# Optimization experiments

Measured on AMD Instinct MI355X. Metric: run time of the kernel, lower is better.

## Reference

```python
import jax, jax.numpy as jnp
import numpy as np
from jax import lax

B, L, LQ, D_IN, ET, H, INIT_EMBED = 16, 256, 64, 32, 128, 4, 8
DIM = 2 * D_IN          # attention value/feature dim (x concat mask)
ETK = ET // H           # per-head time-embedding dim


def _lin(key, fan_in, shape):
    b = 1.0 / np.sqrt(fan_in)
    return jax.random.uniform(key, shape, jnp.float32, -b, b)


def setup_inputs() -> dict:
    key = jax.random.key(0)
    ks = jax.random.split(key, 24)
    inp = {
        "x": jax.random.normal(ks[0], (B, L, D_IN), jnp.float32),
        "time_steps": jnp.sort(jax.random.uniform(ks[1], (B, L), jnp.float32), axis=-1),
        "mask": (jax.random.uniform(ks[2], (B, L, D_IN)) > 0.5).astype(jnp.float32),
        "query": jnp.linspace(0.0, 1.0, LQ, dtype=jnp.float32),
        # time embedding: Linear(1,1) and Linear(1, ET-1)
        "w_lin": _lin(ks[3], 1, (1,)), "b_lin": _lin(ks[4], 1, (1,)),
        "w_per": _lin(ks[5], 1, (ET - 1,)), "b_per": _lin(ks[6], 1, (ET - 1,)),
        # attention projections (stored as (in,out))
        "Wq": _lin(ks[7], ET, (ET, ET)), "bq": _lin(ks[8], ET, (ET,)),
        "Wk": _lin(ks[9], ET, (ET, ET)), "bk": _lin(ks[10], ET, (ET,)),
        "Wo": _lin(ks[11], H * DIM, (H * DIM, ET)), "bo": _lin(ks[12], H * DIM, (ET,)),
        # vanilla RNN (tanh)
        "W_ih": _lin(ks[13], ET, (ET, ET)), "b_ih": _lin(ks[14], ET, (ET,)),
        "W_hh": _lin(ks[15], ET, (ET, ET)), "b_hh": _lin(ks[16], ET, (ET,)),
        "r1_w": _lin(ks[17], ET, (ET, 128)), "r1_b": _lin(ks[17], ET, (128,)),
        "r2_w": _lin(ks[18], 128, (128, 128)), "r2_b": _lin(ks[18], 128, (128,)),
        "r3_w": _lin(ks[19], 128, (128, ET)), "r3_b": _lin(ks[19], 128, (ET,)),
        "r4_w": _lin(ks[20], ET, (ET, INIT_EMBED)), "r4_b": _lin(ks[20], ET, (INIT_EMBED,)),
    }
    return inp


def reference(x, time_steps, mask, query,
              w_lin, b_lin, w_per, b_per,
              Wq, bq, Wk, bk, Wo, bo,
              W_ih, b_ih, W_hh, b_hh,
              r1_w, r1_b, r2_w, r2_b, r3_w, r3_b, r4_w, r4_b):
    def time_embed(tt):  # (...,) -> (..., ET)
        tt = tt[..., None]
        return jnp.concatenate([tt * w_lin + b_lin,
                                jnp.sin(tt * w_per + b_per)], axis=-1)

    xc = jnp.concatenate([x, mask], axis=-1)          # (B,L,DIM) value
    m2 = jnp.concatenate([mask, mask], axis=-1)       # (B,L,DIM)

    kemb = time_embed(time_steps)                     # (B,L,ET)
    qemb = time_embed(query)                          # (LQ,ET)

    q = (qemb @ Wq + bq).reshape(LQ, H, ETK).transpose(1, 0, 2)       # (H,LQ,ETK)
    k = (kemb @ Wk + bk).reshape(B, L, H, ETK).transpose(0, 2, 1, 3)  # (B,H,L,ETK)

    scores = jnp.einsum('hqe,bhke->bhqk', q, k) / np.sqrt(ETK)        # (B,H,LQ,L)
    # per-feature mask broadcast: (B,H,LQ,L,DIM)
    s5 = jnp.where(m2[:, None, None, :, :] == 0, -1e9, scores[..., None])
    p = jax.nn.softmax(s5, axis=-2)                   # softmax over keys L
    att = jnp.einsum('bhqkd,bkd->bhqd', p, xc)        # (B,H,LQ,DIM)
    att = att.transpose(0, 2, 1, 3).reshape(B, LQ, H * DIM)
    out = att @ Wo + bo                               # (B,LQ,ET)

    # vanilla tanh RNN, return final hidden state
    def step(h, xt):
        h = jnp.tanh(xt @ W_ih + b_ih + h @ W_hh + b_hh)
        return h, None
    h0 = jnp.zeros((B, ET), out.dtype)
    hT, _ = lax.scan(step, h0, out.transpose(1, 0, 2))  # scan over LQ

    y = hT @ r1_w + r1_b
    y = y @ r2_w + r2_b
    y = y @ r3_w + r3_b
    y = y @ r4_w + r4_b                               # (B, INIT_EMBED)
    return y
```

## Files before the change

kernel.cpp:

```cpp
#include <hip/hip_runtime.h>
#include <hip/hip_bf16.h>


#define NB 16
#define NL 256
#define NLQ 64
#define NDIN 32
#define NET 128
#define NH 4
#define NETK 32

#define HPAD 136
#define PAD(i) ((i) + 4 * ((i) >> 6))

typedef float f32x2 __attribute__((ext_vector_type(2)));

__global__ __launch_bounds__(128) void k_embed_proj(
    const float* __restrict__ ts, const float* __restrict__ query,
    const float* __restrict__ mask,
    const float* __restrict__ w_lin, const float* __restrict__ b_lin,
    const float* __restrict__ w_per, const float* __restrict__ b_per,
    const float* __restrict__ Wk, const float* __restrict__ bk,
    const float* __restrict__ Wq, const float* __restrict__ bq,
    float* __restrict__ kproj, float* __restrict__ qproj,
    unsigned* __restrict__ mbg) {
  __shared__ __align__(16) float emb[8 * NET];
  int g = blockIdx.x;
  int j = threadIdx.x;
  if (g >= 520) {
    int b = g - 520;
#pragma unroll
    for (int half = 0; half < 2; half++) {
      int r = j + 128 * half;
      const float4* mr4 = (const float4*)(mask + (size_t)(b * NL + r) * NDIN);
      unsigned bits = 0;
#pragma unroll
      for (int u = 0; u < 8; u++) {
        float4 m = mr4[u];
        bits |= (m.x != 0.f ? 1u : 0u) << (4 * u);
        bits |= (m.y != 0.f ? 1u : 0u) << (4 * u + 1);
        bits |= (m.z != 0.f ? 1u : 0u) << (4 * u + 2);
        bits |= (m.w != 0.f ? 1u : 0u) << (4 * u + 3);
      }
      mbg[b * NL + r] = bits;
    }
    return;
  }
  bool isQ = (g >= 512);
  int base = (isQ ? g - 512 : g) * 8;
  float wl_ = w_lin[0], bl_ = b_lin[0];
  float wp = (j > 0) ? w_per[j - 1] : 0.f;
  float bp = (j > 0) ? b_per[j - 1] : 0.f;
#pragma unroll
  for (int rr = 0; rr < 8; rr++) {
    float t = isQ ? query[base + rr] : ts[base + rr];
    emb[rr * NET + j] = (j == 0) ? (t * wl_ + bl_) : sinf(t * wp + bp);
  }
  __syncthreads();
  const float* W = isQ ? Wq : Wk;
  float bias = isQ ? bq[j] : bk[j];
  float acc[8];
#pragma unroll
  for (int rr = 0; rr < 8; rr++) acc[rr] = bias;
#pragma unroll 2
  for (int i = 0; i < NET; i += 4) {
    float w0 = W[(size_t)i * NET + j];
    float w1 = W[(size_t)(i + 1) * NET + j];
    float w2 = W[(size_t)(i + 2) * NET + j];
    float w3 = W[(size_t)(i + 3) * NET + j];
#pragma unroll
    for (int rr = 0; rr < 8; rr++) {
      float4 e4 = *(const float4*)&emb[rr * NET + i];
      acc[rr] += e4.x * w0 + e4.y * w1 + e4.z * w2 + e4.w * w3;
    }
  }
  float* dst = isQ ? qproj : kproj;
#pragma unroll
  for (int rr = 0; rr < 8; rr++) dst[(size_t)(base + rr) * NET + j] = acc[rr];
}

__global__ __launch_bounds__(256) void k_attn(
    const float* __restrict__ x, const unsigned* __restrict__ mbg,
    const float* __restrict__ qproj, const float* __restrict__ kproj,
    float* __restrict__ att) {
  const float SC = 0.17677669529663687f;
  int blk = blockIdx.x;
  int qg = blk & 15;
  int h  = (blk >> 4) & 3;
  int b  = blk >> 6;
  int t  = threadIdx.x;

  __shared__ __align__(16) float es4[NL * 4];
  __shared__ float part[3 * 32 * 9];

  {
    int k = t;
    float kr[NETK];
    const float4* kp =
        (const float4*)(kproj + (size_t)(b * NL + k) * NET + h * NETK);
#pragma unroll
    for (int i = 0; i < 8; i++) {
      float4 v = kp[i];
      kr[4 * i] = v.x; kr[4 * i + 1] = v.y;
      kr[4 * i + 2] = v.z; kr[4 * i + 3] = v.w;
    }
    float ev[4];
#pragma unroll
    for (int qq = 0; qq < 4; qq++) {
      const float* qv = qproj + (size_t)(qg * 4 + qq) * NET + h * NETK;
      float s0 = 0.f, s1 = 0.f;
#pragma unroll
      for (int i = 0; i < NETK; i += 2) {
        s0 += qv[i] * kr[i];
        s1 += qv[i + 1] * kr[i + 1];
      }
      ev[qq] = __expf((s0 + s1) * SC);
    }
    *(float4*)&es4[k * 4] = make_float4(ev[0], ev[1], ev[2], ev[3]);
  }
  __syncthreads();

  int kq = t >> 5, c = t & 31;
  f32x2 den01 = {0.f, 0.f}, den23 = {0.f, 0.f};
  f32x2 num01 = {0.f, 0.f}, num23 = {0.f, 0.f};
  float sumx = 0.f;
  {
    const float* xb = x + (size_t)b * NL * NDIN;
    const unsigned* mbb = mbg + b * NL;
    int k0 = kq * 32;
#pragma unroll 4
    for (int kk = 0; kk < 32; kk++) {
      int k = k0 + kk;
      float4 e4 = *(const float4*)&es4[k * 4];
      float xv = xb[(size_t)k * NDIN + c];
      float mv = ((mbb[k] >> c) & 1u) ? 1.f : 0.f;
      sumx += xv;
      f32x2 e01 = (f32x2){e4.x, e4.y} * mv;
      f32x2 e23 = (f32x2){e4.z, e4.w} * mv;
      den01 += e01;
      den23 += e23;
      num01 += e01 * xv;
      num23 += e23 * xv;
    }
  }
  float den[4] = {den01.x, den01.y, den23.x, den23.y};
  float num[4] = {num01.x, num01.y, num23.x, num23.y};
  sumx += __shfl_xor(sumx, 32, 64);
#pragma unroll
  for (int q = 0; q < 4; q++) {
    den[q] += __shfl_xor(den[q], 32, 64);
    num[q] += __shfl_xor(num[q], 32, 64);
  }
  {
    int w = t >> 6, lane = t & 63;
    if (w > 0 && lane < 32) {
      float* p = &part[((w - 1) * 32 + c) * 9];
#pragma unroll
      for (int q = 0; q < 4; q++) { p[q] = den[q]; p[4 + q] = num[q]; }
      p[8] = sumx;
    }
  }
  __syncthreads();

  if (t < 32) {
#pragma unroll
    for (int ww = 0; ww < 3; ww++) {
      const float* p = &part[(ww * 32 + t) * 9];
#pragma unroll
      for (int q = 0; q < 4; q++) { den[q] += p[q]; num[q] += p[4 + q]; }
      sumx += p[8];
    }
    float meanx = sumx * (1.f / 256.f);
#pragma unroll
    for (int qq = 0; qq < 4; qq++) {
      bool any = (den[qq] > 0.f);
      float* ao =
          att + (size_t)(((b * NLQ + qg * 4 + qq) * NH) + h) * 64;
      ao[t]      = any ? (num[qq] / den[qq]) : meanx;
      ao[32 + t] = any ? 1.f : 0.f;
    }
  }
}

__global__ __launch_bounds__(128) void k_out_xw(
    const float* __restrict__ att,
    const float* __restrict__ Wo, const float* __restrict__ bo,
    const float* __restrict__ Wih, const float* __restrict__ bih,
    const float* __restrict__ bhh, float* __restrict__ XW) {
  int r = blockIdx.x;
  int j = threadIdx.x;
  __shared__ __align__(16) float arow[NH * 64];
  __shared__ __align__(16) float orow[NET];
  arow[j]       = att[(size_t)r * 256 + j];
  arow[j + 128] = att[(size_t)r * 256 + 128 + j];
  __syncthreads();
  float a0 = bo[j], a1 = 0.f, a2 = 0.f, a3 = 0.f;
#pragma unroll 4
  for (int u = 0; u < 256; u += 4) {
    float4 av = *(const float4*)&arow[u];
    a0 += av.x * Wo[(size_t)u * NET + j];
    a1 += av.y * Wo[(size_t)(u + 1) * NET + j];
    a2 += av.z * Wo[(size_t)(u + 2) * NET + j];
    a3 += av.w * Wo[(size_t)(u + 3) * NET + j];
  }
  orow[j] = (a0 + a1) + (a2 + a3);
  __syncthreads();
  float b0 = bih[j] + bhh[j], b1 = 0.f, b2 = 0.f, b3 = 0.f;
#pragma unroll 4
  for (int e = 0; e < NET; e += 4) {
    float4 ov = *(const float4*)&orow[e];
    b0 += ov.x * Wih[(size_t)e * NET + j];
    b1 += ov.y * Wih[(size_t)(e + 1) * NET + j];
    b2 += ov.z * Wih[(size_t)(e + 2) * NET + j];
    b3 += ov.w * Wih[(size_t)(e + 3) * NET + j];
  }
  XW[(size_t)r * NET + j] = (b0 + b1) + (b2 + b3);
}

__device__ __forceinline__ void layer128(const float* src_lds,
                                         const float* __restrict__ W,
                                         const float* __restrict__ bvec,
                                         float* dst_lds, int j, int s) {
  const float4* h4 = (const float4*)(src_lds + s * 68);
  float a0 = 0.f, a1 = 0.f, a2 = 0.f, a3 = 0.f;
#pragma unroll
  for (int i = 0; i < 16; i++) {
    float4 hv = h4[i];
    int base = (s * 64 + 4 * i) * NET + j;
    a0 += hv.x * W[base];
    a1 += hv.y * W[base + NET];
    a2 += hv.z * W[base + 2 * NET];
    a3 += hv.w * W[base + 3 * NET];
  }
  float acc = (a0 + a1) + (a2 + a3);
  acc += __shfl_xor(acc, 1, 64);
  if (s == 0) dst_lds[PAD(j)] = acc + bvec[j];
}

__global__ __launch_bounds__(256, 1) void k_rnn(
    const float* __restrict__ XW, const float* __restrict__ Whh,
    const float* __restrict__ r1w, const float* __restrict__ r1b,
    const float* __restrict__ r2w, const float* __restrict__ r2b,
    const float* __restrict__ r3w, const float* __restrict__ r3b,
    const float* __restrict__ r4w, const float* __restrict__ r4b,
    float* __restrict__ out) {
  int b = blockIdx.x;
  int tid = threadIdx.x;
  int s = tid & 1;
  int j = tid >> 1;
  __shared__ float xwl[NLQ * NET];
  __shared__ float hb[2][HPAD];
  __shared__ float tmp[HPAD];
  {
    const float4* src = (const float4*)(XW + (size_t)b * NLQ * NET);
    float4* dst = (float4*)xwl;
#pragma unroll
    for (int u = 0; u < 8; u++) dst[tid + 256 * u] = src[tid + 256 * u];
  }
  f32x2 w2[32];
#pragma unroll
  for (int i = 0; i < 32; i++) {
    w2[i].x = Whh[(s * 64 + 2 * i) * NET + j];
    w2[i].y = Whh[(s * 64 + 2 * i + 1) * NET + j];
  }
  if (tid < 128) hb[0][PAD(tid)] = 0.f;
  __syncthreads();
  for (int t = 0; t < NLQ; t++) {
    float xwv = xwl[t * NET + j];
    const float4* h4 = (const float4*)&hb[t & 1][s * 68];
    f32x2 accA = {0.f, 0.f}, accB = {0.f, 0.f};
#pragma unroll
    for (int i = 0; i < 16; i++) {
      float4 hv = h4[i];
      accA += (f32x2){hv.x, hv.y} * w2[2 * i];
      accB += (f32x2){hv.z, hv.w} * w2[2 * i + 1];
    }
    float acc = (accA.x + accA.y) + (accB.x + accB.y);
    acc += __shfl_xor(acc, 1, 64);
    if (s == 0) {
      float z = acc + xwv;
      float e2 = __expf(2.f * z);
      hb[(t + 1) & 1][PAD(j)] = 1.f - 2.f / (e2 + 1.f);
    }
    __syncthreads();
  }
  layer128(hb[0], r1w, r1b, tmp, j, s);
  __syncthreads();
  layer128(tmp, r2w, r2b, hb[1], j, s);
  __syncthreads();
  layer128(hb[1], r3w, r3b, hb[0], j, s);
  __syncthreads();
  if (tid < 64) {
    int jj = tid >> 3, p = tid & 7;
    float y = 0.f;
#pragma unroll
    for (int i = 0; i < 16; i++) {
      int ii = p * 16 + i;
      y += hb[0][PAD(ii)] * r4w[ii * 8 + jj];
    }
    y += __shfl_xor(y, 1, 64);
    y += __shfl_xor(y, 2, 64);
    y += __shfl_xor(y, 4, 64);
    if (p == 0) out[b * 8 + jj] = y + r4b[jj];
  }
}

extern "C" void kernel_launch(void* const* d_in, const int* in_sizes, int n_in,
                              void* d_out, int out_size, void* d_ws, size_t ws_size,
                              hipStream_t stream) {
  const float* x     = (const float*)d_in[0];
  const float* ts    = (const float*)d_in[1];
  const float* mask  = (const float*)d_in[2];
  const float* query = (const float*)d_in[3];
  const float* w_lin = (const float*)d_in[4];
  const float* b_lin = (const float*)d_in[5];
  const float* w_per = (const float*)d_in[6];
  const float* b_per = (const float*)d_in[7];
  const float* Wq    = (const float*)d_in[8];
  const float* bq    = (const float*)d_in[9];
  const float* Wk    = (const float*)d_in[10];
  const float* bk    = (const float*)d_in[11];
  const float* Wo    = (const float*)d_in[12];
  const float* bo    = (const float*)d_in[13];
  const float* Wih   = (const float*)d_in[14];
  const float* bih   = (const float*)d_in[15];
  const float* Whh   = (const float*)d_in[16];
  const float* bhh   = (const float*)d_in[17];
  const float* r1w   = (const float*)d_in[18];
  const float* r1b   = (const float*)d_in[19];
  const float* r2w   = (const float*)d_in[20];
  const float* r2b   = (const float*)d_in[21];
  const float* r3w   = (const float*)d_in[22];
  const float* r3b   = (const float*)d_in[23];
  const float* r4w   = (const float*)d_in[24];
  const float* r4b   = (const float*)d_in[25];
  float* out = (float*)d_out;

  float* ws    = (float*)d_ws;
  float* kproj = ws;
  float* qproj = ws + 524288;
  float* att   = ws + 532480;
  float* XW    = ws + 794624;
  unsigned* mbg = (unsigned*)(ws + 925696);

  k_embed_proj<<<536, 128, 0, stream>>>(
      ts, query, mask, w_lin, b_lin, w_per, b_per, Wk, bk, Wq, bq,
      kproj, qproj, mbg);
  k_attn<<<NB * NH * 16, 256, 0, stream>>>(x, mbg, qproj, kproj, att);
  k_out_xw<<<NB * NLQ, 128, 0, stream>>>(att, Wo, bo, Wih, bih, bhh, XW);
  k_rnn<<<NB, 256, 0, stream>>>(XW, Whh, r1w, r1b, r2w, r2b, r3w, r3b,
                                r4w, r4b, out);
}
```

Before: 173.3 us.

## Use packed f32x2 FMA in projections and split RNN step over four lanes

Rewrites the dot-product inner loops of the projection, attention-score and output/input-weight kernels to use two-wide float vector accumulators, which can map to packed FMA instructions. The recurrent kernel moves from 256 to 512 threads, so each hidden unit's recurrent dot product is split across four lanes with 32 weights each instead of two lanes with 64, and the partial sums are combined with an extra shuffle. The aim is to shorten the serial per-timestep latency of the 64-step recurrence. In exchange there is one more shuffle per step, a barrier across twice as many threads each step, and the regressor layers now run on half the block while the rest idles.

```diff
diff --git a/kernel.cpp b/kernel.cpp
--- a/kernel.cpp
+++ b/kernel.cpp
@@ -59,24 +59,24 @@
   __syncthreads();
   const float* W = isQ ? Wq : Wk;
   float bias = isQ ? bq[j] : bk[j];
-  float acc[8];
-#pragma unroll
-  for (int rr = 0; rr < 8; rr++) acc[rr] = bias;
+  f32x2 acc2[8];
+#pragma unroll
+  for (int rr = 0; rr < 8; rr++) acc2[rr] = (f32x2){bias, 0.f};
 #pragma unroll 2
   for (int i = 0; i < NET; i += 4) {
-    float w0 = W[(size_t)i * NET + j];
-    float w1 = W[(size_t)(i + 1) * NET + j];
-    float w2 = W[(size_t)(i + 2) * NET + j];
-    float w3 = W[(size_t)(i + 3) * NET + j];
+    f32x2 wA = {W[(size_t)i * NET + j], W[(size_t)(i + 1) * NET + j]};
+    f32x2 wB = {W[(size_t)(i + 2) * NET + j], W[(size_t)(i + 3) * NET + j]};
 #pragma unroll
     for (int rr = 0; rr < 8; rr++) {
       float4 e4 = *(const float4*)&emb[rr * NET + i];
-      acc[rr] += e4.x * w0 + e4.y * w1 + e4.z * w2 + e4.w * w3;
+      acc2[rr] += (f32x2){e4.x, e4.y} * wA;
+      acc2[rr] += (f32x2){e4.z, e4.w} * wB;
     }
   }
   float* dst = isQ ? qproj : kproj;
 #pragma unroll
-  for (int rr = 0; rr < 8; rr++) dst[(size_t)(base + rr) * NET + j] = acc[rr];
+  for (int rr = 0; rr < 8; rr++)
+    dst[(size_t)(base + rr) * NET + j] = acc2[rr].x + acc2[rr].y;
 }
 
 __global__ __launch_bounds__(256) void k_attn(
@@ -108,13 +108,11 @@
 #pragma unroll
     for (int qq = 0; qq < 4; qq++) {
       const float* qv = qproj + (size_t)(qg * 4 + qq) * NET + h * NETK;
-      float s0 = 0.f, s1 = 0.f;
-#pragma unroll
-      for (int i = 0; i < NETK; i += 2) {
-        s0 += qv[i] * kr[i];
-        s1 += qv[i + 1] * kr[i + 1];
-      }
-      ev[qq] = __expf((s0 + s1) * SC);
+      f32x2 s2 = {0.f, 0.f};
+#pragma unroll
+      for (int i = 0; i < NETK; i += 2)
+        s2 += (f32x2){qv[i], qv[i + 1]} * (f32x2){kr[i], kr[i + 1]};
+      ev[qq] = __expf((s2.x + s2.y) * SC);
     }
     *(float4*)&es4[k * 4] = make_float4(ev[0], ev[1], ev[2], ev[3]);
   }
@@ -194,27 +192,27 @@
   arow[j]       = att[(size_t)r * 256 + j];
   arow[j + 128] = att[(size_t)r * 256 + 128 + j];
   __syncthreads();
-  float a0 = bo[j], a1 = 0.f, a2 = 0.f, a3 = 0.f;
+  f32x2 A = {bo[j], 0.f}, B = {0.f, 0.f};
 #pragma unroll 4
   for (int u = 0; u < 256; u += 4) {
     float4 av = *(const float4*)&arow[u];
-    a0 += av.x * Wo[(size_t)u * NET + j];
-    a1 += av.y * Wo[(size_t)(u + 1) * NET + j];
-    a2 += av.z * Wo[(size_t)(u + 2) * NET + j];
-    a3 += av.w * Wo[(size_t)(u + 3) * NET + j];
-  }
-  orow[j] = (a0 + a1) + (a2 + a3);
-  __syncthreads();
-  float b0 = bih[j] + bhh[j], b1 = 0.f, b2 = 0.f, b3 = 0.f;
+    A += (f32x2){av.x, av.y} *
+         (f32x2){Wo[(size_t)u * NET + j], Wo[(size_t)(u + 1) * NET + j]};
+    B += (f32x2){av.z, av.w} *
+         (f32x2){Wo[(size_t)(u + 2) * NET + j], Wo[(size_t)(u + 3) * NET + j]};
+  }
+  orow[j] = (A.x + A.y) + (B.x + B.y);
+  __syncthreads();
+  f32x2 C = {bih[j] + bhh[j], 0.f}, D = {0.f, 0.f};
 #pragma unroll 4
   for (int e = 0; e < NET; e += 4) {
     float4 ov = *(const float4*)&orow[e];
-    b0 += ov.x * Wih[(size_t)e * NET + j];
-    b1 += ov.y * Wih[(size_t)(e + 1) * NET + j];
-    b2 += ov.z * Wih[(size_t)(e + 2) * NET + j];
-    b3 += ov.w * Wih[(size_t)(e + 3) * NET + j];
-  }
-  XW[(size_t)r * NET + j] = (b0 + b1) + (b2 + b3);
+    C += (f32x2){ov.x, ov.y} *
+         (f32x2){Wih[(size_t)e * NET + j], Wih[(size_t)(e + 1) * NET + j]};
+    D += (f32x2){ov.z, ov.w} *
+         (f32x2){Wih[(size_t)(e + 2) * NET + j], Wih[(size_t)(e + 3) * NET + j]};
+  }
+  XW[(size_t)r * NET + j] = (C.x + C.y) + (D.x + D.y);
 }
 
 __device__ __forceinline__ void layer128(const float* src_lds,
@@ -237,7 +235,7 @@
   if (s == 0) dst_lds[PAD(j)] = acc + bvec[j];
 }
 
-__global__ __launch_bounds__(256, 1) void k_rnn(
+__global__ __launch_bounds__(512, 1) void k_rnn(
     const float* __restrict__ XW, const float* __restrict__ Whh,
     const float* __restrict__ r1w, const float* __restrict__ r1b,
     const float* __restrict__ r2w, const float* __restrict__ r2b,
@@ -246,8 +244,8 @@
     float* __restrict__ out) {
   int b = blockIdx.x;
   int tid = threadIdx.x;
-  int s = tid & 1;
-  int j = tid >> 1;
+  int s = tid & 3;
+  int j = tid >> 2;
   __shared__ float xwl[NLQ * NET];
   __shared__ float hb[2][HPAD];
   __shared__ float tmp[HPAD];
@@ -255,28 +253,31 @@
     const float4* src = (const float4*)(XW + (size_t)b * NLQ * NET);
     float4* dst = (float4*)xwl;
 #pragma unroll
-    for (int u = 0; u < 8; u++) dst[tid + 256 * u] = src[tid + 256 * u];
-  }
-  f32x2 w2[32];
-#pragma unroll
-  for (int i = 0; i < 32; i++) {
-    w2[i].x = Whh[(s * 64 + 2 * i) * NET + j];
-    w2[i].y = Whh[(s * 64 + 2 * i + 1) * NET + j];
+    for (int u = 0; u < 4; u++) dst[tid + 512 * u] = src[tid + 512 * u];
+  }
+  int qoff = s * 32;
+  f32x2 w2[16];
+#pragma unroll
+  for (int i = 0; i < 16; i++) {
+    w2[i].x = Whh[(size_t)(qoff + 2 * i) * NET + j];
+    w2[i].y = Whh[(size_t)(qoff + 2 * i + 1) * NET + j];
   }
   if (tid < 128) hb[0][PAD(tid)] = 0.f;
   __syncthreads();
+  int loff = qoff + 4 * (s >> 1);
   for (int t = 0; t < NLQ; t++) {
     float xwv = xwl[t * NET + j];
-    const float4* h4 = (const float4*)&hb[t & 1][s * 68];
+    const float4* h4 = (const float4*)&hb[t & 1][loff];
     f32x2 accA = {0.f, 0.f}, accB = {0.f, 0.f};
 #pragma unroll
-    for (int i = 0; i < 16; i++) {
+    for (int i = 0; i < 8; i++) {
       float4 hv = h4[i];
       accA += (f32x2){hv.x, hv.y} * w2[2 * i];
       accB += (f32x2){hv.z, hv.w} * w2[2 * i + 1];
     }
     float acc = (accA.x + accA.y) + (accB.x + accB.y);
     acc += __shfl_xor(acc, 1, 64);
+    acc += __shfl_xor(acc, 2, 64);
     if (s == 0) {
       float z = acc + xwv;
       float e2 = __expf(2.f * z);
@@ -284,11 +285,12 @@
     }
     __syncthreads();
   }
-  layer128(hb[0], r1w, r1b, tmp, j, s);
-  __syncthreads();
-  layer128(tmp, r2w, r2b, hb[1], j, s);
-  __syncthreads();
-  layer128(hb[1], r3w, r3b, hb[0], j, s);
+  int s2 = tid & 1, j2 = tid >> 1;
+  if (tid < 256) layer128(hb[0], r1w, r1b, tmp, j2, s2);
+  __syncthreads();
+  if (tid < 256) layer128(tmp, r2w, r2b, hb[1], j2, s2);
+  __syncthreads();
+  if (tid < 256) layer128(hb[1], r3w, r3b, hb[0], j2, s2);
   __syncthreads();
   if (tid < 64) {
     int jj = tid >> 3, p = tid & 7;
@@ -348,6 +350,6 @@
       kproj, qproj, mbg);
   k_attn<<<NB * NH * 16, 256, 0, stream>>>(x, mbg, qproj, kproj, att);
   k_out_xw<<<NB * NLQ, 128, 0, stream>>>(att, Wo, bo, Wih, bih, bhh, XW);
-  k_rnn<<<NB, 256, 0, stream>>>(XW, Whh, r1w, r1b, r2w, r2b, r3w, r3b,
+  k_rnn<<<NB, 512, 0, stream>>>(XW, Whh, r1w, r1b, r2w, r2b, r3w, r3b,
                                 r4w, r4b, out);
 }
```

After: 172.1 us. No clear change (-0.7%).
